# Performance work log

Hardware: AMD Instinct MI355X
Metric: run time of the kernel (lower is better)

## Reference

```python
import jax, jax.numpy as jnp
import numpy as np

N, C, H, W = 32, 128, 56, 56
K, KS = 256, 3
STRIDE, PAD = 1, 1


def setup_inputs() -> dict:
    key = jax.random.key(0)
    k1, k2, k3 = jax.random.split(key, 3)
    x = jax.random.normal(k1, (N, C, H, W), dtype=jnp.float32)
    stdv = 1.0 / np.sqrt(C * KS * KS)
    weight = jax.random.uniform(k2, (K, C, KS, KS), dtype=jnp.float32, minval=-stdv, maxval=stdv)
    bias = jax.random.uniform(k3, (K,), dtype=jnp.float32, minval=-stdv, maxval=stdv)
    return {"input": x, "weight": weight, "bias": bias}


def _binarize(t):
    # sign(t) * mean(|t|)  (XNOR-Net style scaled binarization)
    return jnp.sign(t) * jnp.mean(jnp.abs(t))


def reference(input, weight, bias):
    bx = _binarize(input)
    bw = _binarize(weight)
    out = jax.lax.conv_general_dilated(
        bx, bw,
        window_strides=(STRIDE, STRIDE),
        padding=[(PAD, PAD), (PAD, PAD)],
        dimension_numbers=("NCHW", "OIHW", "NCHW"),
    )
    return out + bias[None, :, None, None]
```

## Files before the change

kernel.cpp:

```cpp
#include <hip/hip_runtime.h>
#include <hip/hip_bf16.h>
#include <cstdint>

#define NB   32
#define CIN  128
#define HH   56
#define WW   56
#define KOUT 256
#define HWS  (HH*WW)
#define NHW  (NB*HWS)
#define XCNT ((float)(NB*CIN*HWS))
#define WCNT ((float)(KOUT*CIN*9))

__global__ __launch_bounds__(64) void zero_sums_kernel(float* sums) {
    if (threadIdx.x < 2) sums[threadIdx.x] = 0.0f;
}

__device__ __forceinline__ void block_reduce_add(float v, float* dst) {
    #pragma unroll
    for (int off = 32; off > 0; off >>= 1) v += __shfl_down(v, off);
    __shared__ float ws4[4];
    int lane = threadIdx.x & 63, wid = threadIdx.x >> 6;
    if (lane == 0) ws4[wid] = v;
    __syncthreads();
    if (threadIdx.x == 0) {
        float s = ws4[0];
        int nw = (blockDim.x + 63) >> 6;
        for (int i = 1; i < nw; i++) s += ws4[i];
        atomicAdd(dst, s);
    }
}

__global__ __launch_bounds__(256) void pack_x_kernel(const float* __restrict__ x,
                                                     uint32_t* __restrict__ xpackw,
                                                     float* __restrict__ sums) {
    int j   = blockIdx.x / (NHW / 256);
    int idx = (blockIdx.x - j * (NHW / 256)) * 256 + threadIdx.x;
    int n  = idx / HWS;
    int hw = idx - n * HWS;
    const float* p = x + (size_t)n * CIN * HWS + (size_t)(j * 32) * HWS + hw;
    float asum = 0.0f;
    uint32_t bits = 0;
    #pragma unroll
    for (int t = 0; t < 32; t++) {
        float v = p[(size_t)t * HWS];
        asum += fabsf(v);
        bits |= (v > 0.0f ? 1u : 0u) << t;
    }
    xpackw[idx * 4 + j] = bits;
    block_reduce_add(asum, &sums[0]);
}

__global__ __launch_bounds__(256) void pack_w_kernel(const float* __restrict__ wgt,
                                                     uint32_t* __restrict__ wpackTw,
                                                     float* __restrict__ sums) {
    int k   = threadIdx.x;
    int tap = blockIdx.x >> 2;
    int j   = blockIdx.x & 3;
    const float* p = wgt + (size_t)k * CIN * 9 + (size_t)(j * 32) * 9 + tap;
    float asum = 0.0f;
    uint32_t bits = 0;
    #pragma unroll
    for (int t = 0; t < 32; t++) {
        float v = p[(size_t)t * 9];
        asum += fabsf(v);
        bits |= (v > 0.0f ? 1u : 0u) << t;
    }
    wpackTw[(tap * KOUT + k) * 4 + j] = bits;
    block_reduce_add(asum, &sums[1]);
}

__global__ __launch_bounds__(256) void conv_kernel(const uint4* __restrict__ xpack,
                                                   const uint4* __restrict__ wpackT,
                                                   const float* __restrict__ sums,
                                                   const float* __restrict__ bias,
                                                   float* __restrict__ out) {
    __shared__ uint4 xl[58 * 3];
    __shared__ float sbuf[KOUT * 10];

    int tid = threadIdx.x;
    int bid = blockIdx.x;
    int n = bid / HH, h = bid - n * HH;
    int lane = tid & 63, wid = tid >> 6;

    uint4 wq[9];
    #pragma unroll
    for (int t = 0; t < 9; t++) wq[t] = wpackT[t * KOUT + tid];

    for (int e = tid; e < 58 * 3; e += 256) {
        int col = e / 3, row = e - col * 3;
        int rw = col - 1, hy = h - 1 + row;
        uint4 q = make_uint4(0, 0, 0, 0);
        if (rw >= 0 && rw < WW && hy >= 0 && hy < HH)
            q = xpack[(n * HH + hy) * WW + rw];
        xl[e] = q;
    }

    float scale = (sums[0] * (1.0f / XCNT)) * (sums[1] * (1.0f / WCNT));
    float m2s   = -2.0f * scale;
    float cbase = 1152.0f * scale + bias[tid];

    int pw[9];
    #pragma unroll
    for (int t = 0; t < 9; t++)
        pw[t] = __popc(wq[t].x) + __popc(wq[t].y) + __popc(wq[t].z) + __popc(wq[t].w);
    int cs0 = pw[0] + pw[3] + pw[6];
    int cs2 = pw[2] + pw[5] + pw[8];
    int rterm = 0, cc0 = 0, cc2 = 0;
    if (h == 0)        { rterm = 2*(pw[0]+pw[1]+pw[2]) - 384; cc0 = 128 - 2*pw[0]; cc2 = 128 - 2*pw[2]; }
    else if (h == HH-1){ rterm = 2*(pw[6]+pw[7]+pw[8]) - 384; cc0 = 128 - 2*pw[6]; cc2 = 128 - 2*pw[8]; }
    float CB  = cbase + scale * (float)rterm;
    float F0  = CB + scale * (float)(2*cs0 - 384 + cc0);
    float F55 = CB + scale * (float)(2*cs2 - 384 + cc2);

    __syncthreads();

    float* sb = &sbuf[tid * 10];
    uint4 xs[6][3];

#define LOADCOL(S, C) { xs[S][0] = xl[(C)*3+0]; xs[S][1] = xl[(C)*3+1]; xs[S][2] = xl[(C)*3+2]; }
#define MINC(c) ((c) > 57 ? 57 : (c))
#define T4(a, q, wt) a += __popc((q).x^(wt).x) + __popc((q).y^(wt).y) + __popc((q).z^(wt).z) + __popc((q).w^(wt).w);
#define FLUSH(C) { \
    _Pragma("unroll") \
    for (int r = 0; r < 4; r++) { \
        int kl = r * 16 + (lane >> 2); \
        int wo = (lane & 3) * 2; \
        float2 v2 = *(float2*)&sbuf[(wid * 64 + kl) * 10 + wo]; \
        *(float2*)&out[(size_t)(n * KOUT + wid * 64 + kl) * HWS + h * WW + (C) * 8 + wo] = v2; \
    } }
#define BODY(L, M, R, W, PC) { \
    int a0 = 0, a1 = 0, a2 = 0; \
    T4(a0, xs[L][0], wq[0]) T4(a0, xs[M][0], wq[1]) T4(a0, xs[R][0], wq[2]) \
    T4(a1, xs[L][1], wq[3]) T4(a1, xs[M][1], wq[4]) T4(a1, xs[R][1], wq[5]) \
    T4(a2, xs[L][2], wq[6]) T4(a2, xs[M][2], wq[7]) T4(a2, xs[R][2], wq[8]) \
    LOADCOL(L, PC) \
    sb[(W) & 7] = fmaf(m2s, (float)(a0 + a1 + a2), CB); \
    if (((W) & 7) == 7) FLUSH((W) >> 3) \
}

    LOADCOL(0, 0) LOADCOL(1, 1) LOADCOL(2, 2)
    LOADCOL(3, 3) LOADCOL(4, 4) LOADCOL(5, 5)

    {
        int a0 = cs0, a1 = 0, a2 = 0;
        T4(a0, xs[1][0], wq[1]) T4(a0, xs[2][0], wq[2])
        T4(a1, xs[1][1], wq[4]) T4(a1, xs[2][1], wq[5])
        T4(a2, xs[1][2], wq[7]) T4(a2, xs[2][2], wq[8])
        LOADCOL(0, 6)
        sb[0] = fmaf(m2s, (float)(a0 + a1 + a2), F0);
    }

    #pragma unroll 1
    for (int w = 1; w <= 49; w += 6) {
        BODY(1, 2, 3, w,     MINC(w + 6))
        BODY(2, 3, 4, w + 1, MINC(w + 7))
        BODY(3, 4, 5, w + 2, MINC(w + 8))
        BODY(4, 5, 0, w + 3, MINC(w + 9))
        BODY(5, 0, 1, w + 4, MINC(w + 10))
        BODY(0, 1, 2, w + 5, MINC(w + 11))
    }

    {
        int a0 = cs2, a1 = 0, a2 = 0;
        T4(a0, xs[1][0], wq[0]) T4(a0, xs[2][0], wq[1])
        T4(a1, xs[1][1], wq[3]) T4(a1, xs[2][1], wq[4])
        T4(a2, xs[1][2], wq[6]) T4(a2, xs[2][2], wq[7])
        sb[7] = fmaf(m2s, (float)(a0 + a1 + a2), F55);
        FLUSH(6)
    }
}

extern "C" void kernel_launch(void* const* d_in, const int* in_sizes, int n_in,
                              void* d_out, int out_size, void* d_ws, size_t ws_size,
                              hipStream_t stream) {
    const float* x    = (const float*)d_in[0];
    const float* wgt  = (const float*)d_in[1];
    const float* bias = (const float*)d_in[2];
    float* out = (float*)d_out;

    float* sums   = (float*)d_ws;
    uint4* xpack  = (uint4*)((char*)d_ws + 256);
    uint4* wpackT = (uint4*)((char*)d_ws + 256 + (size_t)NHW * 16);

    hipLaunchKernelGGL(zero_sums_kernel, dim3(1), dim3(64), 0, stream, sums);
    hipLaunchKernelGGL(pack_w_kernel, dim3(36), dim3(256), 0, stream, wgt, (uint32_t*)wpackT, sums);
    hipLaunchKernelGGL(pack_x_kernel, dim3(4 * NHW / 256), dim3(256), 0, stream, x, (uint32_t*)xpack, sums);
    hipLaunchKernelGGL(conv_kernel, dim3(NB * HH), dim3(256), 0, stream, xpack, wpackT, sums, bias, out);
}
```

Measured before the change: 110.0 us.

## Pad packed input rows and split conv into single-wave blocks streaming directly from global

The packed input is stored with zero-padded top and bottom rows, so the conv kernel drops its shared-memory staging and bounds checks and instead prefetches columns straight from global memory into a rotating register window. Each conv block is now one 64-lane wave handling a quarter of the output channels, with four times as many blocks and no block-level barrier. The aim is to remove the LDS staging and __syncthreads cost and to raise occupancy and scheduling flexibility. In exchange, each input row segment is fetched by four blocks instead of one, relying on cache hits, and the padding rows must be zeroed by an extra init pass.

```diff
diff --git a/kernel.cpp b/kernel.cpp
--- a/kernel.cpp
+++ b/kernel.cpp
@@ -1,5 +1,4 @@
 #include <hip/hip_runtime.h>
-#include <hip/hip_bf16.h>
 #include <cstdint>
 
 #define NB   32
@@ -9,11 +8,18 @@
 #define KOUT 256
 #define HWS  (HH*WW)
 #define NHW  (NB*HWS)
+#define PADH 58
 #define XCNT ((float)(NB*CIN*HWS))
 #define WCNT ((float)(KOUT*CIN*9))
 
-__global__ __launch_bounds__(64) void zero_sums_kernel(float* sums) {
-    if (threadIdx.x < 2) sums[threadIdx.x] = 0.0f;
+__global__ __launch_bounds__(256) void init_kernel(uint4* __restrict__ xpad,
+                                                   float* __restrict__ sums) {
+    int idx = blockIdx.x * 256 + threadIdx.x;
+    if (idx < 2) sums[idx] = 0.0f;
+    int n = idx / 112, rem = idx - n * 112;
+    int prow = (rem < 56) ? 0 : 57;
+    int w = rem % 56;
+    xpad[(n * PADH + prow) * WW + w] = make_uint4(0, 0, 0, 0);
 }
 
 __device__ __forceinline__ void block_reduce_add(float v, float* dst) {
@@ -32,12 +38,14 @@
 }
 
 __global__ __launch_bounds__(256) void pack_x_kernel(const float* __restrict__ x,
-                                                     uint32_t* __restrict__ xpackw,
+                                                     uint32_t* __restrict__ xpadw,
                                                      float* __restrict__ sums) {
     int j   = blockIdx.x / (NHW / 256);
     int idx = (blockIdx.x - j * (NHW / 256)) * 256 + threadIdx.x;
     int n  = idx / HWS;
     int hw = idx - n * HWS;
+    int h  = hw / WW;
+    int w  = hw - h * WW;
     const float* p = x + (size_t)n * CIN * HWS + (size_t)(j * 32) * HWS + hw;
     float asum = 0.0f;
     uint32_t bits = 0;
@@ -47,7 +55,7 @@
         asum += fabsf(v);
         bits |= (v > 0.0f ? 1u : 0u) << t;
     }
-    xpackw[idx * 4 + j] = bits;
+    xpadw[(((n * PADH + h + 1) * WW + w) << 2) + j] = bits;
     block_reduce_add(asum, &sums[0]);
 }
 
@@ -70,35 +78,36 @@
     block_reduce_add(asum, &sums[1]);
 }
 
-__global__ __launch_bounds__(256) void conv_kernel(const uint4* __restrict__ xpack,
-                                                   const uint4* __restrict__ wpackT,
-                                                   const float* __restrict__ sums,
-                                                   const float* __restrict__ bias,
-                                                   float* __restrict__ out) {
-    __shared__ uint4 xl[58 * 3];
-    __shared__ float sbuf[KOUT * 10];
+__global__ __launch_bounds__(64, 4) void conv_kernel(const uint4* __restrict__ xpad,
+                                                     const uint4* __restrict__ wpackT,
+                                                     const float* __restrict__ sums,
+                                                     const float* __restrict__ bias,
+                                                     float* __restrict__ out) {
+    __shared__ float sbuf[64 * 10];
 
-    int tid = threadIdx.x;
+    int l   = threadIdx.x;
     int bid = blockIdx.x;
-    int n = bid / HH, h = bid - n * HH;
-    int lane = tid & 63, wid = tid >> 6;
+    int kg  = bid & 3;
+    int nh  = bid >> 2;
+    int n   = nh / HH, h = nh - n * HH;
+    int k   = kg * 64 + l;
 
     uint4 wq[9];
     #pragma unroll
-    for (int t = 0; t < 9; t++) wq[t] = wpackT[t * KOUT + tid];
+    for (int t = 0; t < 9; t++) wq[t] = wpackT[t * KOUT + k];
 
-    for (int e = tid; e < 58 * 3; e += 256) {
-        int col = e / 3, row = e - col * 3;
-        int rw = col - 1, hy = h - 1 + row;
-        uint4 q = make_uint4(0, 0, 0, 0);
-        if (rw >= 0 && rw < WW && hy >= 0 && hy < HH)
-            q = xpack[(n * HH + hy) * WW + rw];
-        xl[e] = q;
+    const uint4* P = xpad + (size_t)(n * PADH + h) * WW;
+
+    uint4 xs[4][3];
+#define PF(S, OFF) { xs[S][0] = PB[OFF]; xs[S][1] = PB[56 + (OFF)]; xs[S][2] = PB[112 + (OFF)]; }
+    {
+        const uint4* PB = P;
+        PF(0, 0) PF(1, 1) PF(2, 2) PF(3, 3)
     }
 
     float scale = (sums[0] * (1.0f / XCNT)) * (sums[1] * (1.0f / WCNT));
     float m2s   = -2.0f * scale;
-    float cbase = 1152.0f * scale + bias[tid];
+    float cbase = 1152.0f * scale + bias[k];
 
     int pw[9];
     #pragma unroll
@@ -113,59 +122,54 @@
     float F0  = CB + scale * (float)(2*cs0 - 384 + cc0);
     float F55 = CB + scale * (float)(2*cs2 - 384 + cc2);
 
-    __syncthreads();
+    float* sb = &sbuf[l * 10];
+    int fbase = (l >> 2) * 10 + (l & 3) * 2;
+    float* o0 = out + ((size_t)(n * KOUT + kg * 64 + (l >> 2)) * HWS + h * WW + (l & 3) * 2);
+    float* o1 = o0 + (size_t)16 * HWS;
+    float* o2 = o1 + (size_t)16 * HWS;
+    float* o3 = o2 + (size_t)16 * HWS;
 
-    float* sb = &sbuf[tid * 10];
-    uint4 xs[6][3];
-
-#define LOADCOL(S, C) { xs[S][0] = xl[(C)*3+0]; xs[S][1] = xl[(C)*3+1]; xs[S][2] = xl[(C)*3+2]; }
-#define MINC(c) ((c) > 57 ? 57 : (c))
 #define T4(a, q, wt) a += __popc((q).x^(wt).x) + __popc((q).y^(wt).y) + __popc((q).z^(wt).z) + __popc((q).w^(wt).w);
 #define FLUSH(C) { \
-    _Pragma("unroll") \
-    for (int r = 0; r < 4; r++) { \
-        int kl = r * 16 + (lane >> 2); \
-        int wo = (lane & 3) * 2; \
-        float2 v2 = *(float2*)&sbuf[(wid * 64 + kl) * 10 + wo]; \
-        *(float2*)&out[(size_t)(n * KOUT + wid * 64 + kl) * HWS + h * WW + (C) * 8 + wo] = v2; \
-    } }
-#define BODY(L, M, R, W, PC) { \
+    *(float2*)(o0 + (C) * 8) = *(float2*)&sbuf[fbase];       \
+    *(float2*)(o1 + (C) * 8) = *(float2*)&sbuf[fbase + 160]; \
+    *(float2*)(o2 + (C) * 8) = *(float2*)&sbuf[fbase + 320]; \
+    *(float2*)(o3 + (C) * 8) = *(float2*)&sbuf[fbase + 480]; \
+}
+#define CORE(J) \
     int a0 = 0, a1 = 0, a2 = 0; \
-    T4(a0, xs[L][0], wq[0]) T4(a0, xs[M][0], wq[1]) T4(a0, xs[R][0], wq[2]) \
-    T4(a1, xs[L][1], wq[3]) T4(a1, xs[M][1], wq[4]) T4(a1, xs[R][1], wq[5]) \
-    T4(a2, xs[L][2], wq[6]) T4(a2, xs[M][2], wq[7]) T4(a2, xs[R][2], wq[8]) \
-    LOADCOL(L, PC) \
-    sb[(W) & 7] = fmaf(m2s, (float)(a0 + a1 + a2), CB); \
-    if (((W) & 7) == 7) FLUSH((W) >> 3) \
-}
-
-    LOADCOL(0, 0) LOADCOL(1, 1) LOADCOL(2, 2)
-    LOADCOL(3, 3) LOADCOL(4, 4) LOADCOL(5, 5)
+    T4(a0, xs[(J)&3][0], wq[0]) T4(a0, xs[((J)+1)&3][0], wq[1]) T4(a0, xs[((J)+2)&3][0], wq[2]) \
+    T4(a1, xs[(J)&3][1], wq[3]) T4(a1, xs[((J)+1)&3][1], wq[4]) T4(a1, xs[((J)+2)&3][1], wq[5]) \
+    T4(a2, xs[(J)&3][2], wq[6]) T4(a2, xs[((J)+1)&3][2], wq[7]) T4(a2, xs[((J)+2)&3][2], wq[8])
+#define BODY(J)   { CORE(J) PF((J)&3, (J)+4) sb[((J)+1)&7] = fmaf(m2s, (float)(a0+a1+a2), CB); }
+#define BODYNP(J) { CORE(J) sb[((J)+1)&7] = fmaf(m2s, (float)(a0+a1+a2), CB); }
 
     {
         int a0 = cs0, a1 = 0, a2 = 0;
-        T4(a0, xs[1][0], wq[1]) T4(a0, xs[2][0], wq[2])
-        T4(a1, xs[1][1], wq[4]) T4(a1, xs[2][1], wq[5])
-        T4(a2, xs[1][2], wq[7]) T4(a2, xs[2][2], wq[8])
-        LOADCOL(0, 6)
+        T4(a0, xs[0][0], wq[1]) T4(a0, xs[1][0], wq[2])
+        T4(a1, xs[0][1], wq[4]) T4(a1, xs[1][1], wq[5])
+        T4(a2, xs[0][2], wq[7]) T4(a2, xs[1][2], wq[8])
         sb[0] = fmaf(m2s, (float)(a0 + a1 + a2), F0);
     }
 
-    #pragma unroll 1
-    for (int w = 1; w <= 49; w += 6) {
-        BODY(1, 2, 3, w,     MINC(w + 6))
-        BODY(2, 3, 4, w + 1, MINC(w + 7))
-        BODY(3, 4, 5, w + 2, MINC(w + 8))
-        BODY(4, 5, 0, w + 3, MINC(w + 9))
-        BODY(5, 0, 1, w + 4, MINC(w + 10))
-        BODY(0, 1, 2, w + 5, MINC(w + 11))
+    {
+        const uint4* PB = P;
+        #pragma unroll 1
+        for (int i = 0; i < 6; i++) {
+            BODY(0) BODY(1) BODY(2) BODY(3) BODY(4) BODY(5)
+            BODY(6)
+            FLUSH(i)
+            BODY(7)
+            PB += 8;
+        }
+        BODY(0) BODY(1) BODY(2) BODY(3) BODYNP(4) BODYNP(5)
     }
 
     {
         int a0 = cs2, a1 = 0, a2 = 0;
-        T4(a0, xs[1][0], wq[0]) T4(a0, xs[2][0], wq[1])
-        T4(a1, xs[1][1], wq[3]) T4(a1, xs[2][1], wq[4])
-        T4(a2, xs[1][2], wq[6]) T4(a2, xs[2][2], wq[7])
+        T4(a0, xs[2][0], wq[0]) T4(a0, xs[3][0], wq[1])
+        T4(a1, xs[2][1], wq[3]) T4(a1, xs[3][1], wq[4])
+        T4(a2, xs[2][2], wq[6]) T4(a2, xs[3][2], wq[7])
         sb[7] = fmaf(m2s, (float)(a0 + a1 + a2), F55);
         FLUSH(6)
     }
@@ -180,11 +184,11 @@
     float* out = (float*)d_out;
 
     float* sums   = (float*)d_ws;
-    uint4* xpack  = (uint4*)((char*)d_ws + 256);
-    uint4* wpackT = (uint4*)((char*)d_ws + 256 + (size_t)NHW * 16);
+    uint4* xpad   = (uint4*)((char*)d_ws + 256);
+    uint4* wpackT = (uint4*)((char*)d_ws + 256 + (size_t)NB * PADH * WW * 16);
 
-    hipLaunchKernelGGL(zero_sums_kernel, dim3(1), dim3(64), 0, stream, sums);
+    hipLaunchKernelGGL(init_kernel, dim3(14), dim3(256), 0, stream, xpad, sums);
     hipLaunchKernelGGL(pack_w_kernel, dim3(36), dim3(256), 0, stream, wgt, (uint32_t*)wpackT, sums);
-    hipLaunchKernelGGL(pack_x_kernel, dim3(4 * NHW / 256), dim3(256), 0, stream, x, (uint32_t*)xpack, sums);
-    hipLaunchKernelGGL(conv_kernel, dim3(NB * HH), dim3(256), 0, stream, xpack, wpackT, sums, bias, out);
+    hipLaunchKernelGGL(pack_x_kernel, dim3(4 * NHW / 256), dim3(256), 0, stream, x, (uint32_t*)xpad, sums);
+    hipLaunchKernelGGL(conv_kernel, dim3(NB * HH * 4), dim3(64), 0, stream, xpad, wpackT, sums, bias, out);
 }
```

Result: slower. 113.1 us (+2.9%).
